# Kernel optimization log

Hardware: AMD Instinct MI355X
Metric: run time of the kernel (lower is better)

Reference implementation:

```python
import jax, jax.numpy as jnp
import numpy as np

B, D_IN = 8192, 1024
E, T = 8, 4
H1, H2, H3 = 1024, 512, 256


def setup_inputs() -> dict:
    key = jax.random.key(0)
    ks = jax.random.split(key, 8)
    s1 = 1.0 / np.sqrt(D_IN)
    s2 = 1.0 / np.sqrt(H1)
    s3 = 1.0 / np.sqrt(H2)
    return {
        "x": jax.random.normal(ks[0], (B, D_IN), jnp.float32),
        "W1": jax.random.normal(ks[1], (E, D_IN, H1), jnp.float32) * s1,
        "b1": jnp.zeros((E, H1), jnp.float32),
        "W2": jax.random.normal(ks[2], (E, H1, H2), jnp.float32) * s2,
        "b2": jnp.zeros((E, H2), jnp.float32),
        "W3": jax.random.normal(ks[3], (E, H2, H3), jnp.float32) * s3,
        "b3": jnp.zeros((E, H3), jnp.float32),
        "gate_w": jax.random.normal(ks[4], (D_IN, T * E), jnp.float32) * 0.05,
    }


def reference(x, W1, b1, W2, b2, W3, b3, gate_w):
    # Expert MLPs, vectorized over experts: h = relu(x @ W + b)
    h = jax.nn.relu(jnp.einsum("bi,eio->beo", x, W1) + b1[None])      # [B,E,H1]
    h = jax.nn.relu(jnp.einsum("beh,eho->beo", h, W2) + b2[None])     # [B,E,H2]
    h = jax.nn.relu(jnp.einsum("beh,eho->beo", h, W3) + b3[None])     # [B,E,H3]
    expert_outputs = jnp.transpose(h, (0, 2, 1))                       # [B,D_out,E]

    # Gates: logits [B, T*E] -> [B,T,E], softmax over experts, -> [B,E,T]
    logits = (x @ gate_w).reshape(B, T, E)
    gates = jax.nn.softmax(logits, axis=2)
    gates = jnp.transpose(gates, (0, 2, 1))                            # [B,E,T]

    mmoe_output = jnp.matmul(expert_outputs, gates)                    # [B,D_out,T]
    # unstack along task axis -> tuple of T [B, D_out] arrays
    return tuple(mmoe_output[:, :, t] for t in range(T))
```

## Files before the change

### kernel.cpp

```cpp
#include <hip/hip_runtime.h>


#define B_ROWS 8192
#define D_IN   1024
#define NEXP   8
#define NTASK  4
#define H1     1024
#define H2     512
#define H3     256

typedef __attribute__((ext_vector_type(8))) short bf16x8;
typedef __attribute__((ext_vector_type(4))) float f32x4;

__device__ __forceinline__ unsigned short f2bf(float f) {
    union { float f; unsigned int u; } x; x.f = f;
    unsigned int r = x.u + 0x7fffu + ((x.u >> 16) & 1u);
    return (unsigned short)(r >> 16);
}
__device__ __forceinline__ float bf2f(unsigned short u) {
    union { unsigned int u; float f; } x; x.u = ((unsigned int)u) << 16;
    return x.f;
}

__device__ __forceinline__ void gload_lds16(const void* gptr, void* lptr) {
    __builtin_amdgcn_global_load_lds(
        (__attribute__((address_space(1))) void*)gptr,
        (__attribute__((address_space(3))) void*)lptr,
        16, 0, 0);
}

struct __align__(8) us4 { unsigned short x, y, z, w; };

__global__ void convert_x_kernel(const float* __restrict__ x,
                                 unsigned short* __restrict__ xb) {
    int i = blockIdx.x * blockDim.x + threadIdx.x;
    float4 v = ((const float4*)x)[i];
    us4 o;
    o.x = f2bf(v.x); o.y = f2bf(v.y); o.z = f2bf(v.z); o.w = f2bf(v.w);
    ((us4*)xb)[i] = o;
}

__global__ void transpose_convert_kernel(const float* __restrict__ W,
                                         unsigned short* __restrict__ Wt,
                                         int K, int N) {
    __shared__ float tile[32][33];
    const int e = blockIdx.z;
    const float* We = W + (size_t)e * K * N;
    unsigned short* Wte = Wt + (size_t)e * K * N;
    const int k0 = blockIdx.x * 32, n0 = blockIdx.y * 32;
    const int tx = threadIdx.x, ty = threadIdx.y;
#pragma unroll
    for (int i = 0; i < 4; ++i)
        tile[ty + i * 8][tx] = We[(size_t)(k0 + ty + i * 8) * N + n0 + tx];
    __syncthreads();
#pragma unroll
    for (int i = 0; i < 4; ++i)
        Wte[(size_t)(n0 + ty + i * 8) * K + k0 + tx] = f2bf(tile[tx][ty + i * 8]);
}

__global__ __launch_bounds__(256, 2) void gemm_bias_relu_kernel(
    const unsigned short* __restrict__ A, long long Aes,
    const unsigned short* __restrict__ Bt, long long Bes,
    const float* __restrict__ bias, long long bias_es,
    unsigned short* __restrict__ C, long long Ces,
    int M, int N, int K) {
    __shared__ __align__(16) unsigned short sA[256 * 64];
    __shared__ __align__(16) unsigned short sB[128 * 64];

    const int tid  = threadIdx.x;
    const int lane = tid & 63;
    const int w    = tid >> 6;
    const int wr   = w >> 1, wc = w & 1;
    const int quad = lane >> 4, l15 = lane & 15;
    const int r8   = lane >> 3;
    const int c8   = lane & 7;
    const int gchunk = c8 ^ r8;

    const int e  = blockIdx.z;
    const int m0 = blockIdx.x * 256;
    const int n0 = blockIdx.y * 128;

    A    += (size_t)e * Aes;
    Bt   += (size_t)e * Bes;
    bias += (size_t)e * bias_es;
    C    += (size_t)e * Ces;

    f32x4 acc[8][4] = {};

    const int swz = (l15 & 7);

    for (int k0 = 0; k0 < K; k0 += 64) {
#pragma unroll
        for (int q = 0; q < 8; ++q) {
            const int row = w * 64 + q * 8 + r8;
            gload_lds16(A + (size_t)(m0 + row) * K + k0 + gchunk * 8,
                        &sA[row * 64 + c8 * 8]);
        }
#pragma unroll
        for (int q = 0; q < 4; ++q) {
            const int row = w * 32 + q * 8 + r8;
            gload_lds16(Bt + (size_t)(n0 + row) * K + k0 + gchunk * 8,
                        &sB[row * 64 + c8 * 8]);
        }
        __syncthreads();

#pragma unroll
        for (int s = 0; s < 2; ++s) {
            const int cs = ((s * 4 + quad) ^ swz) * 8;
            bf16x8 af[8], bfv[4];
#pragma unroll
            for (int j = 0; j < 4; ++j)
                bfv[j] = *(const bf16x8*)&sB[(wc * 64 + j * 16 + l15) * 64 + cs];
#pragma unroll
            for (int i = 0; i < 8; ++i)
                af[i] = *(const bf16x8*)&sA[(wr * 128 + i * 16 + l15) * 64 + cs];
#pragma unroll
            for (int i = 0; i < 8; ++i)
#pragma unroll
                for (int j = 0; j < 4; ++j)
                    acc[i][j] = __builtin_amdgcn_mfma_f32_16x16x32_bf16(
                        af[i], bfv[j], acc[i][j], 0, 0, 0);
        }
        __syncthreads();
    }

#pragma unroll
    for (int j = 0; j < 4; ++j) {
        const int col = n0 + wc * 64 + j * 16 + l15;
        const float bv = bias[col];
#pragma unroll
        for (int i = 0; i < 8; ++i) {
#pragma unroll
            for (int r = 0; r < 4; ++r) {
                const int row = m0 + wr * 128 + i * 16 + quad * 4 + r;
                float v = acc[i][j][r] + bv;
                v = v > 0.f ? v : 0.f;
                C[(size_t)row * N + col] = f2bf(v);
            }
        }
    }
}

__global__ void gates_kernel(const float* __restrict__ x,
                             const float* __restrict__ gw,
                             float* __restrict__ gates) {
    const int tid = threadIdx.x;
    const int o = tid & 31;
    const int r = tid >> 5;
    const int b = blockIdx.x * 8 + r;
    const float* xr = x + (size_t)b * D_IN;
    float acc = 0.f;
    for (int k = 0; k < D_IN; k += 4) {
        float4 xv = *(const float4*)&xr[k];
        acc += xv.x * gw[(k + 0) * 32 + o];
        acc += xv.y * gw[(k + 1) * 32 + o];
        acc += xv.z * gw[(k + 2) * 32 + o];
        acc += xv.w * gw[(k + 3) * 32 + o];
    }
    float m = acc;
    m = fmaxf(m, __shfl_xor(m, 1));
    m = fmaxf(m, __shfl_xor(m, 2));
    m = fmaxf(m, __shfl_xor(m, 4));
    float ex = __expf(acc - m);
    float s = ex;
    s += __shfl_xor(s, 1);
    s += __shfl_xor(s, 2);
    s += __shfl_xor(s, 4);
    gates[(size_t)b * 32 + o] = ex / s;
}

__global__ void combine_kernel(const unsigned short* __restrict__ h3,
                               const float* __restrict__ gates,
                               float* __restrict__ out) {
    __shared__ float g[32];
    const int b = blockIdx.x;
    const int d = threadIdx.x;
    if (d < 32) g[d] = gates[(size_t)b * 32 + d];
    __syncthreads();
    float acc[NTASK] = {0.f, 0.f, 0.f, 0.f};
#pragma unroll
    for (int e = 0; e < NEXP; ++e) {
        const float h = bf2f(h3[((size_t)e * B_ROWS + b) * H3 + d]);
#pragma unroll
        for (int t = 0; t < NTASK; ++t) acc[t] += h * g[t * 8 + e];
    }
#pragma unroll
    for (int t = 0; t < NTASK; ++t)
        out[((size_t)t * B_ROWS + b) * H3 + d] = acc[t];
}

#define OFF_XBF 0u
#define OFF_W1T 16777216u
#define OFF_W2T 33554432u
#define OFF_W3T 41943040u
#define OFF_G   44040192u
#define OFF_H1  45088768u
#define OFF_H2  179306496u
#define OFF_H3  45088768u

extern "C" void kernel_launch(void* const* d_in, const int* in_sizes, int n_in,
                              void* d_out, int out_size, void* d_ws, size_t ws_size,
                              hipStream_t stream) {
    const float* x  = (const float*)d_in[0];
    const float* W1 = (const float*)d_in[1];
    const float* b1 = (const float*)d_in[2];
    const float* W2 = (const float*)d_in[3];
    const float* b2 = (const float*)d_in[4];
    const float* W3 = (const float*)d_in[5];
    const float* b3 = (const float*)d_in[6];
    const float* gw = (const float*)d_in[7];
    float* out = (float*)d_out;
    char* ws = (char*)d_ws;

    unsigned short* xbf = (unsigned short*)(ws + OFF_XBF);
    unsigned short* w1t = (unsigned short*)(ws + OFF_W1T);
    unsigned short* w2t = (unsigned short*)(ws + OFF_W2T);
    unsigned short* w3t = (unsigned short*)(ws + OFF_W3T);
    float*          gts = (float*)(ws + OFF_G);
    unsigned short* h1  = (unsigned short*)(ws + OFF_H1);
    unsigned short* h2  = (unsigned short*)(ws + OFF_H2);
    unsigned short* h3  = (unsigned short*)(ws + OFF_H3);

    convert_x_kernel<<<dim3((B_ROWS * D_IN) / 4 / 256), dim3(256), 0, stream>>>(x, xbf);
    transpose_convert_kernel<<<dim3(D_IN / 32, H1 / 32, NEXP), dim3(32, 8), 0, stream>>>(W1, w1t, D_IN, H1);
    transpose_convert_kernel<<<dim3(H1 / 32, H2 / 32, NEXP), dim3(32, 8), 0, stream>>>(W2, w2t, H1, H2);
    transpose_convert_kernel<<<dim3(H2 / 32, H3 / 32, NEXP), dim3(32, 8), 0, stream>>>(W3, w3t, H2, H3);

    gates_kernel<<<dim3(B_ROWS / 8), dim3(256), 0, stream>>>(x, gw, gts);

    gemm_bias_relu_kernel<<<dim3(B_ROWS / 256, H1 / 128, NEXP), dim3(256), 0, stream>>>(
        xbf, 0LL,
        w1t, (long long)H1 * D_IN,
        b1, (long long)H1,
        h1, (long long)B_ROWS * H1,
        B_ROWS, H1, D_IN);
    gemm_bias_relu_kernel<<<dim3(B_ROWS / 256, H2 / 128, NEXP), dim3(256), 0, stream>>>(
        h1, (long long)B_ROWS * H1,
        w2t, (long long)H2 * H1,
        b2, (long long)H2,
        h2, (long long)B_ROWS * H2,
        B_ROWS, H2, H1);
    gemm_bias_relu_kernel<<<dim3(B_ROWS / 256, H3 / 128, NEXP), dim3(256), 0, stream>>>(
        h2, (long long)B_ROWS * H2,
        w3t, (long long)H3 * H2,
        b3, (long long)H3,
        h3, (long long)B_ROWS * H3,
        B_ROWS, H3, H2);

    combine_kernel<<<dim3(B_ROWS), dim3(256), 0, stream>>>(h3, gts, out);
}
```

Before: 455.7 us.

## Load A fragments directly from global and double-buffer B tiles in LDS

The GEMM kernel stops staging the A tile in shared memory and has each wave read its A fragments straight from global memory into registers. The B tile is double-buffered in LDS so the next k-slice is prefetched while the current one is consumed, which also removes one barrier per iteration. The goal is to overlap global loads with MFMA work and cut LDS traffic and footprint. In exchange, A reads become 16-byte per-lane global loads with row strides, so they are poorly coalesced. Their latency is exposed right before the MFMAs, and rows shared between the two waves in a column pair are fetched twice.

```diff
diff --git a/kernel.cpp b/kernel.cpp
--- a/kernel.cpp
+++ b/kernel.cpp
@@ -64,8 +64,7 @@
     const float* __restrict__ bias, long long bias_es,
     unsigned short* __restrict__ C, long long Ces,
     int M, int N, int K) {
-    __shared__ __align__(16) unsigned short sA[256 * 64];
-    __shared__ __align__(16) unsigned short sB[128 * 64];
+    __shared__ __align__(16) unsigned short sB[2][128 * 64];
 
     const int tid  = threadIdx.x;
     const int lane = tid & 63;
@@ -85,43 +84,54 @@
     bias += (size_t)e * bias_es;
     C    += (size_t)e * Ces;
 
+    const unsigned short* Arow = A + (size_t)(m0 + wr * 128 + l15) * K + quad * 8;
+
+    const unsigned short* Bbase = Bt + (size_t)(n0 + w * 32 + r8) * K + gchunk * 8;
+    unsigned short* sBw = &sB[0][(w * 32 + r8) * 64 + c8 * 8];
+
     f32x4 acc[8][4] = {};
-
-    const int swz = (l15 & 7);
-
-    for (int k0 = 0; k0 < K; k0 += 64) {
-#pragma unroll
-        for (int q = 0; q < 8; ++q) {
-            const int row = w * 64 + q * 8 + r8;
-            gload_lds16(A + (size_t)(m0 + row) * K + k0 + gchunk * 8,
-                        &sA[row * 64 + c8 * 8]);
+    const int swz = l15 & 7;
+    const int niter = K >> 6;
+
+#pragma unroll
+    for (int q = 0; q < 4; ++q)
+        gload_lds16(Bbase + (size_t)(q * 8) * K, sBw + q * 8 * 64);
+
+    for (int it = 0; it < niter; ++it) {
+        __syncthreads();
+
+        bf16x8 af[2][8];
+        const size_t ka = (size_t)it * 64;
+#pragma unroll
+        for (int s = 0; s < 2; ++s)
+#pragma unroll
+            for (int i = 0; i < 8; ++i)
+                af[s][i] = *(const bf16x8*)(Arow + (size_t)(i * 16) * K + ka + s * 32);
+
+        if (it + 1 < niter) {
+            const int buf = (it + 1) & 1;
+            const size_t koff = (size_t)(it + 1) << 6;
+#pragma unroll
+            for (int q = 0; q < 4; ++q)
+                gload_lds16(Bbase + (size_t)(q * 8) * K + koff,
+                            sBw + buf * (128 * 64) + q * 8 * 64);
         }
-#pragma unroll
-        for (int q = 0; q < 4; ++q) {
-            const int row = w * 32 + q * 8 + r8;
-            gload_lds16(Bt + (size_t)(n0 + row) * K + k0 + gchunk * 8,
-                        &sB[row * 64 + c8 * 8]);
-        }
-        __syncthreads();
-
+
+        const unsigned short* b_ = sB[it & 1];
 #pragma unroll
         for (int s = 0; s < 2; ++s) {
             const int cs = ((s * 4 + quad) ^ swz) * 8;
-            bf16x8 af[8], bfv[4];
+            bf16x8 bfv[4];
 #pragma unroll
             for (int j = 0; j < 4; ++j)
-                bfv[j] = *(const bf16x8*)&sB[(wc * 64 + j * 16 + l15) * 64 + cs];
-#pragma unroll
-            for (int i = 0; i < 8; ++i)
-                af[i] = *(const bf16x8*)&sA[(wr * 128 + i * 16 + l15) * 64 + cs];
+                bfv[j] = *(const bf16x8*)&b_[(wc * 64 + j * 16 + l15) * 64 + cs];
 #pragma unroll
             for (int i = 0; i < 8; ++i)
 #pragma unroll
                 for (int j = 0; j < 4; ++j)
                     acc[i][j] = __builtin_amdgcn_mfma_f32_16x16x32_bf16(
-                        af[i], bfv[j], acc[i][j], 0, 0, 0);
+                        af[s][i], bfv[j], acc[i][j], 0, 0, 0);
         }
-        __syncthreads();
     }
 
 #pragma unroll
```

Result: slower. 712.3 us (+56.3%).
